# Kernel optimization log

Hardware: AMD Instinct MI355X
Metric: run time of the kernel (lower is better)

The kernel has to match this reference:

```python
import jax, jax.numpy as jnp
import numpy as np
from jax import lax

N, S, K, V, C, D, NH, NB, HD = 4, 1024, 4, 32000, 1000, 512, 8, 6, 2048
DH = D // NH
CAP = round((S // K) * 1.0)  # expert capacity = Seq//K * capacity_factor


def setup_inputs() -> dict:
    key = jax.random.key(0)
    ks = jax.random.split(key, 12)
    nrm = lambda k, shape: jax.random.normal(k, shape, dtype=jnp.float32) * 0.02
    return dict(
        x_in=jax.random.randint(ks[0], (N, S), 0, V),
        y_target=jax.random.randint(ks[1], (N, S), 0, C),
        tok_emb=nrm(ks[2], (K, V, D)),
        pos_emb=nrm(ks[3], (K, S, D)),
        ln1_s=jnp.ones((K, NB, D)), ln1_b=jnp.zeros((K, NB, D)),
        Wqkv=nrm(ks[4], (K, NB, D, 3 * D)), bqkv=jnp.zeros((K, NB, 3 * D)),
        Wo=nrm(ks[5], (K, NB, D, D)), bo=jnp.zeros((K, NB, D)),
        ln2_s=jnp.ones((K, NB, D)), ln2_b=jnp.zeros((K, NB, D)),
        W1=nrm(ks[6], (K, NB, D, HD)), b1=jnp.zeros((K, NB, HD)),
        W2=nrm(ks[7], (K, NB, HD, D)), b2=jnp.zeros((K, NB, D)),
        lnf_s=jnp.ones((K, D)), lnf_b=jnp.zeros((K, D)),
        Wcls=nrm(ks[8], (K, D, C)), bcls=jnp.zeros((K, C)),
        Wconf=nrm(ks[9], (K, D, 1)), bconf=jnp.zeros((K, 1)),
    )


def _ln(x, s, b):
    m = x.mean(-1, keepdims=True)
    v = jnp.var(x, axis=-1, keepdims=True)
    return (x - m) * lax.rsqrt(v + 1e-5) * s + b


def reference(x_in, y_target, tok_emb, pos_emb, ln1_s, ln1_b, Wqkv, bqkv, Wo, bo,
              ln2_s, ln2_b, W1, b1, W2, b2, lnf_s, lnf_b, Wcls, bcls, Wconf, bconf):
    causal = jnp.tril(jnp.ones((S, S), dtype=bool))

    def model_fwd(te, pe, l1s, l1b, wqkv, bq, wo, bo_, l2s, l2b, w1, b1_, w2, b2_, lfs, lfb, wc, bc, wcf, bcf):
        x = te[x_in] + pe[None]  # [N,S,D]
        for i in range(NB):
            h = _ln(x, l1s[i], l1b[i])
            qkv = h @ wqkv[i] + bq[i]
            q, k, v = jnp.split(qkv, 3, axis=-1)
            q = q.reshape(N, S, NH, DH); k = k.reshape(N, S, NH, DH); v = v.reshape(N, S, NH, DH)
            att = jnp.einsum('nqhd,nkhd->nhqk', q, k) / np.float32(np.sqrt(DH))
            att = jax.nn.softmax(jnp.where(causal, att, jnp.float32(-1e9)), axis=-1)
            o = jnp.einsum('nhqk,nkhd->nqhd', att, v).reshape(N, S, D)
            x = x + o @ wo[i] + bo_[i]
            h = _ln(x, l2s[i], l2b[i])
            x = x + jax.nn.gelu(h @ w1[i] + b1_[i]) @ w2[i] + b2_[i]
        x = _ln(x, lfs, lfb)
        return x @ wc + bc, x @ wcf + bcf  # logits [N,S,C], confidence [N,S,1]

    clf, conf = jax.vmap(model_fwd)(tok_emb, pos_emb, ln1_s, ln1_b, Wqkv, bqkv, Wo, bo,
                                    ln2_s, ln2_b, W1, b1, W2, b2, lnf_s, lnf_b, Wcls, bcls, Wconf, bconf)
    combined_classifier = jnp.transpose(clf, (1, 0, 2, 3))       # [N,K,S,C]
    combined_confidence = jnp.transpose(conf[..., 0], (1, 0, 2))  # [N,K,S]

    # --- capacity-constrained auction routing on detached logits ---
    logp = jax.nn.log_softmax(lax.stop_gradient(combined_classifier), axis=-1)
    tgt = jnp.broadcast_to(y_target[:, None, :, None], (N, K, S, 1))
    loss = -jnp.take_along_axis(logp, tgt, axis=-1)[..., 0]  # per-token CE, [N,K,S]
    order = jnp.argsort(loss, axis=1, stable=True)            # [N,K,S] models sorted by loss
    order_s = jnp.transpose(order, (2, 0, 1))                 # [S,N,K]
    rows = jnp.arange(N)

    def step(tc, chunk):  # tc: token_count [N,K]; chunk: [N,K]
        tcm = jnp.take_along_axis(tc, chunk, axis=1)
        best = jnp.argmax((tcm < CAP).astype(jnp.float32), axis=1)
        chosen = chunk[rows, best]
        return tc.at[rows, chosen].add(1.0), chosen

    _, chosen = lax.scan(step, jnp.zeros((N, K), dtype=jnp.float32), order_s)
    activated_models_indices = chosen.T  # [N,S]

    mask = jax.nn.one_hot(activated_models_indices, K, dtype=combined_classifier.dtype)  # [N,S,K]
    mask = jnp.transpose(mask, (0, 2, 1))[..., None]  # [N,K,S,1]
    out = (combined_classifier * mask).sum(axis=1)    # [N,S,C]
    return out, combined_confidence, activated_models_indices
```

## Files before the change

### kernel.cpp

```cpp
#include <hip/hip_runtime.h>
#include <hip/hip_bf16.h>

#define N_  4
#define S_  1024
#define K_  4
#define V_  32000
#define C_  1000
#define D_  512
#define NH_ 8
#define NB_ 6
#define HD_ 2048
#define DH_ 64
#define CAP_ 256
#define M_  (N_*S_)

typedef __attribute__((ext_vector_type(8))) short short8_t;
typedef __attribute__((ext_vector_type(4))) float f32x4_t;

#define MFMA16(a,b,c) __builtin_amdgcn_mfma_f32_16x16x32_bf16((a),(b),(c),0,0,0)

#define HSPLANE ((size_t)M_ * D_)
#define WTMAX   ((size_t)524288)

static __device__ __forceinline__ float bfround(float v) {
    unsigned u = __float_as_uint(v);
    u = (u + 0x7FFFu + ((u >> 16) & 1u)) & 0xFFFF0000u;
    return __uint_as_float(u);
}
static __device__ __forceinline__ void split3(float v, unsigned short& a, unsigned short& b, unsigned short& c) {
    const float f0 = bfround(v);      const float r1 = v - f0;
    const float f1 = bfround(r1);     const float f2 = bfround(r1 - f1);
    a = (unsigned short)(__float_as_uint(f0) >> 16);
    b = (unsigned short)(__float_as_uint(f1) >> 16);
    c = (unsigned short)(__float_as_uint(f2) >> 16);
}
static __device__ __forceinline__ float b2f(unsigned short u) {
    return __uint_as_float((unsigned)u << 16);
}

__global__ __launch_bounds__(256) void embed_kernel(const int* __restrict__ x_in,
    const float* __restrict__ tok, const float* __restrict__ pos, float* __restrict__ x)
{
    const int idx = blockIdx.x * 256 + threadIdx.x;
    const int total = M_ * (D_ / 4);
    if (idx >= total) return;
    const int d = (idx & (D_ / 4 - 1)) * 4;
    const int row = idx >> 7;
    const int s = row & (S_ - 1);
    const int t = x_in[row];
    const float4 a = *(const float4*)(tok + (size_t)t * D_ + d);
    const float4 b = *(const float4*)(pos + (size_t)s * D_ + d);
    float4 r; r.x = a.x + b.x; r.y = a.y + b.y; r.z = a.z + b.z; r.w = a.w + b.w;
    *(float4*)(x + (size_t)row * D_ + d) = r;
}

__global__ __launch_bounds__(256) void ln_kernel(const float* __restrict__ x,
    const float* __restrict__ sc, const float* __restrict__ bi, unsigned short* __restrict__ hs)
{
    const int row = blockIdx.x, tid = threadIdx.x;
    const float* xr = x + (size_t)row * D_;
    float v0 = xr[tid], v1 = xr[tid + 256];
    float s1 = v0 + v1;
#pragma unroll
    for (int off = 32; off; off >>= 1) s1 += __shfl_down(s1, off, 64);
    __shared__ float red[8];
    __shared__ float stat[2];
    const int wid = tid >> 6, lane = tid & 63;
    if (lane == 0) red[wid] = s1;
    __syncthreads();
    if (tid == 0) stat[0] = (red[0] + red[1] + red[2] + red[3]) * (1.f / (float)D_);
    __syncthreads();
    const float mean = stat[0];
    const float d0 = v0 - mean, d1 = v1 - mean;
    float s2 = d0 * d0 + d1 * d1;
#pragma unroll
    for (int off = 32; off; off >>= 1) s2 += __shfl_down(s2, off, 64);
    if (lane == 0) red[wid] = s2;
    __syncthreads();
    if (tid == 0) stat[1] = (red[0] + red[1] + red[2] + red[3]) * (1.f / (float)D_);
    __syncthreads();
    const float rstd = rsqrtf(stat[1] + 1e-5f);
    const float o0 = d0 * rstd * sc[tid] + bi[tid];
    const float o1 = d1 * rstd * sc[tid + 256] + bi[tid + 256];
    unsigned short a, b, c;
    const size_t base = (size_t)row * D_ + tid;
    split3(o0, a, b, c);
    hs[base] = a; hs[base + HSPLANE] = b; hs[base + 2 * HSPLANE] = c;
    split3(o1, a, b, c);
    hs[base + 256] = a; hs[base + 256 + HSPLANE] = b; hs[base + 256 + 2 * HSPLANE] = c;
}

__global__ __launch_bounds__(256) void wsplit_kernel(const float* __restrict__ W, int ldw, int NcTrue,
    unsigned short* __restrict__ Wt, size_t bplane, int Kd)
{
    const int tid = threadIdx.x;
    const int n = blockIdx.x * 64 + (tid & 63);
    const int k0 = blockIdx.y * 32 + (tid >> 6) * 8;
    unsigned short q0[8], q1[8], q2[8];
    if (n < NcTrue) {
#pragma unroll
        for (int j = 0; j < 8; ++j) split3(W[(size_t)(k0 + j) * ldw + n], q0[j], q1[j], q2[j]);
    } else {
#pragma unroll
        for (int j = 0; j < 8; ++j) { q0[j] = 0; q1[j] = 0; q2[j] = 0; }
    }
    unsigned short* dst = Wt + (size_t)n * Kd + k0;
    *(uint4*)dst = *(uint4*)&q0[0];
    *(uint4*)(dst + bplane) = *(uint4*)&q1[0];
    *(uint4*)(dst + 2 * bplane) = *(uint4*)&q2[0];
}

template<int MODE>
__global__ __launch_bounds__(256, 2) void gemm64(const unsigned short* __restrict__ A3, size_t aplane,
    const unsigned short* __restrict__ Bt, size_t bplane, const float* __restrict__ bias,
    void* __restrict__ Cv, size_t cplane, int Nc, int ldc)
{
    constexpr int KD = (MODE == 4) ? 1024 : 512;
    __shared__ __align__(16) unsigned short Bs[3][64][40];
    const int tid = threadIdx.x;
    const int gx = gridDim.x;
    const int nwg = gx * gridDim.y;
    const int bid = blockIdx.y * gx + blockIdx.x;
    const int cpx = nwg >> 3;
    const int swz = (bid & 7) * cpx + (bid >> 3);
    const int bm = (swz / gx) * 128, bn = (swz % gx) * 64;
    const int wid = tid >> 6, lane = tid & 63;
    const int wm = (wid >> 1) * 64, wn = (wid & 1) * 32;
    const int lr = lane & 15, lg = lane >> 4;
    const int scol = tid >> 2, skq = tid & 3;
    const unsigned short* Bp0 = Bt + (size_t)(bn + scol) * KD + skq * 8;
    const unsigned short* Ap0 = A3 + (size_t)(bm + wm + lr) * KD + lg * 8;

    f32x4_t acc[4][2] = {};

#pragma unroll
    for (int k0 = 0; k0 < KD; k0 += 32) {
        const uint4 bq0 = *(const uint4*)(Bp0 + k0);
        const uint4 bq1 = *(const uint4*)(Bp0 + bplane + k0);
        const uint4 bq2 = *(const uint4*)(Bp0 + 2 * bplane + k0);
        short8_t af[3][4];
#pragma unroll
        for (int m = 0; m < 4; ++m) {
            const unsigned short* ap = Ap0 + (size_t)m * 16 * KD + k0;
            af[0][m] = *(const short8_t*)ap;
            af[1][m] = *(const short8_t*)(ap + aplane);
            af[2][m] = *(const short8_t*)(ap + 2 * aplane);
        }
        __syncthreads();
        *(uint4*)&Bs[0][scol][skq * 8] = bq0;
        *(uint4*)&Bs[1][scol][skq * 8] = bq1;
        *(uint4*)&Bs[2][scol][skq * 8] = bq2;
        __syncthreads();
        short8_t bg[3][2];
#pragma unroll
        for (int s = 0; s < 3; ++s)
#pragma unroll
            for (int n2 = 0; n2 < 2; ++n2)
                bg[s][n2] = *(const short8_t*)&Bs[s][wn + n2 * 16 + lr][lg * 8];
#pragma unroll
        for (int m = 0; m < 4; ++m)
#pragma unroll
            for (int n2 = 0; n2 < 2; ++n2) {
                f32x4_t c = acc[m][n2];
                c = MFMA16(af[0][m], bg[0][n2], c);
                c = MFMA16(af[0][m], bg[1][n2], c);
                c = MFMA16(af[1][m], bg[0][n2], c);
                c = MFMA16(af[1][m], bg[1][n2], c);
                c = MFMA16(af[0][m], bg[2][n2], c);
                c = MFMA16(af[2][m], bg[0][n2], c);
                acc[m][n2] = c;
            }
    }
#pragma unroll
    for (int m = 0; m < 4; ++m)
#pragma unroll
        for (int n2 = 0; n2 < 2; ++n2) {
            const int col = bn + wn + n2 * 16 + lr;
            if (col >= Nc) continue;
            const float bv = bias ? bias[col] : 0.f;
            const int row0 = bm + wm + m * 16 + lg * 4;
#pragma unroll
            for (int r = 0; r < 4; ++r) {
                float v = acc[m][n2][r] + bv;
                if (MODE == 2) {
                    const float t = v;
                    v = 0.5f * t * (1.f + tanhf(0.7978845608028654f * (t + 0.044715f * t * t * t)));
                    unsigned short a, b, c;
                    split3(v, a, b, c);
                    unsigned short* Cp = (unsigned short*)Cv + (size_t)(row0 + r) * ldc + col;
                    Cp[0] = a; Cp[cplane] = b; Cp[2 * cplane] = c;
                } else {
                    float* cp = (float*)Cv + (size_t)(row0 + r) * ldc + col;
                    if (MODE == 1 || MODE == 4) v += *cp;
                    *cp = v;
                }
            }
        }
}

__global__ __launch_bounds__(256) void rerun_kernel(const unsigned short* __restrict__ A,
    const unsigned short* __restrict__ B0, const float* __restrict__ bias,
    const int* __restrict__ chosen, const int kk, float* __restrict__ out)
{
    __shared__ int anyrow;
    const int tid = threadIdx.x;
    const int bm = blockIdx.y * 128, bn = blockIdx.x * 64;
    if (tid == 0) anyrow = 0;
    __syncthreads();
    if (tid < 128 && chosen[bm + tid] == kk) anyrow = 1;
    __syncthreads();
    if (!anyrow) return;
    const int wid = tid >> 6, lane = tid & 63;
    const int wm = (wid >> 1) * 64, wn = (wid & 1) * 32;
    const int lr = lane & 15, lg = lane >> 4;
    f32x4_t acc[4][2] = {};
#pragma unroll
    for (int k0 = 0; k0 < D_; k0 += 32) {
        short8_t af[4], bg[2];
#pragma unroll
        for (int m = 0; m < 4; ++m)
            af[m] = *(const short8_t*)(A + (size_t)(bm + wm + m * 16 + lr) * D_ + k0 + lg * 8);
#pragma unroll
        for (int n2 = 0; n2 < 2; ++n2)
            bg[n2] = *(const short8_t*)(B0 + (size_t)(bn + wn + n2 * 16 + lr) * D_ + k0 + lg * 8);
#pragma unroll
        for (int m = 0; m < 4; ++m)
#pragma unroll
            for (int n2 = 0; n2 < 2; ++n2)
                acc[m][n2] = MFMA16(af[m], bg[n2], acc[m][n2]);
    }
#pragma unroll
    for (int m = 0; m < 4; ++m)
#pragma unroll
        for (int n2 = 0; n2 < 2; ++n2) {
            const int col = bn + wn + n2 * 16 + lr;
            if (col >= C_) continue;
            const float bv = bias[col];
            const int row0 = bm + wm + m * 16 + lg * 4;
#pragma unroll
            for (int r = 0; r < 4; ++r) {
                const int row = row0 + r;
                if (chosen[row] == kk) out[(size_t)row * C_ + col] = acc[m][n2][r] + bv;
            }
        }
}

__global__ __launch_bounds__(256) void attn_mfma_kernel(const float* __restrict__ qkv, unsigned short* __restrict__ hsO)
{
    __shared__ __align__(16) unsigned short Ks[3][32][72];
    __shared__ __align__(16) unsigned short Vt[3][64][40];
    __shared__ __align__(16) unsigned short Ps[4][3][16][40];
    const int qt = blockIdx.x, hh = blockIdx.y, n = blockIdx.z;
    const int tid = threadIdx.x;
    const int w = tid >> 6, lane = tid & 63;
    const int lr = lane & 15, lg = lane >> 4;
    const size_t rs = 3 * D_;
    const float* base = qkv + (size_t)n * S_ * rs + hh * DH_;

    short8_t qf[3][2];
    {
        const int qrow = qt * 64 + w * 16 + lr;
#pragma unroll
        for (int ks = 0; ks < 2; ++ks) {
            const float* qp = base + (size_t)qrow * rs + ks * 32 + lg * 8;
            float v[8];
            *(float4*)&v[0] = ((const float4*)qp)[0];
            *(float4*)&v[4] = ((const float4*)qp)[1];
#pragma unroll
            for (int j = 0; j < 8; ++j) {
                unsigned short a, b, c;
                split3(v[j], a, b, c);
                qf[0][ks][j] = (short)a; qf[1][ks][j] = (short)b; qf[2][ks][j] = (short)c;
            }
        }
    }

    f32x4_t oacc[4] = {};
    float m_r[4], l_r[4];
#pragma unroll
    for (int r = 0; r < 4; ++r) { m_r[r] = -1e30f; l_r[r] = 0.f; }

    const int ktmax = 2 * qt + 2;
    for (int kt = 0; kt < ktmax; ++kt) {
        __syncthreads();
        {
            const int key = tid & 31, seg = tid >> 5;
            const float* kp = base + (size_t)(kt * 32 + key) * rs + D_ + seg * 8;
            const float* vp = kp + D_;
            float kv[8], vv[8];
            *(float4*)&kv[0] = ((const float4*)kp)[0];
            *(float4*)&kv[4] = ((const float4*)kp)[1];
            *(float4*)&vv[0] = ((const float4*)vp)[0];
            *(float4*)&vv[4] = ((const float4*)vp)[1];
            unsigned short k0a[8], k1a[8], k2a[8];
#pragma unroll
            for (int j = 0; j < 8; ++j) split3(kv[j], k0a[j], k1a[j], k2a[j]);
            *(uint4*)&Ks[0][key][seg * 8] = *(uint4*)&k0a[0];
            *(uint4*)&Ks[1][key][seg * 8] = *(uint4*)&k1a[0];
            *(uint4*)&Ks[2][key][seg * 8] = *(uint4*)&k2a[0];
#pragma unroll
            for (int j = 0; j < 8; ++j) {
                unsigned short a, b, c;
                split3(vv[j], a, b, c);
                Vt[0][seg * 8 + j][key] = a;
                Vt[1][seg * 8 + j][key] = b;
                Vt[2][seg * 8 + j][key] = c;
            }
        }
        __syncthreads();
        f32x4_t sacc[2] = {};
#pragma unroll
        for (int n2 = 0; n2 < 2; ++n2) {
#pragma unroll
            for (int ks = 0; ks < 2; ++ks) {
                short8_t kb0 = *(const short8_t*)&Ks[0][n2 * 16 + lr][ks * 32 + lg * 8];
                short8_t kb1 = *(const short8_t*)&Ks[1][n2 * 16 + lr][ks * 32 + lg * 8];
                short8_t kb2 = *(const short8_t*)&Ks[2][n2 * 16 + lr][ks * 32 + lg * 8];
                f32x4_t c = sacc[n2];
                c = MFMA16(qf[0][ks], kb0, c);
                c = MFMA16(qf[0][ks], kb1, c);
                c = MFMA16(qf[1][ks], kb0, c);
                c = MFMA16(qf[1][ks], kb1, c);
                c = MFMA16(qf[0][ks], kb2, c);
                c = MFMA16(qf[2][ks], kb0, c);
                sacc[n2] = c;
            }
        }
        float p[2][4];
#pragma unroll
        for (int n2 = 0; n2 < 2; ++n2)
#pragma unroll
            for (int r = 0; r < 4; ++r) {
                float s = sacc[n2][r] * 0.125f;
                const int key = kt * 32 + n2 * 16 + lr;
                const int qrow = qt * 64 + w * 16 + lg * 4 + r;
                if (key > qrow) s = -1e30f;
                p[n2][r] = s;
            }
        float scl[4];
#pragma unroll
        for (int r = 0; r < 4; ++r) {
            float tm = fmaxf(p[0][r], p[1][r]);
            tm = fmaxf(tm, __shfl_xor(tm, 1));
            tm = fmaxf(tm, __shfl_xor(tm, 2));
            tm = fmaxf(tm, __shfl_xor(tm, 4));
            tm = fmaxf(tm, __shfl_xor(tm, 8));
            const float mnew = fmaxf(m_r[r], tm);
            scl[r] = expf(m_r[r] - mnew);
            m_r[r] = mnew;
        }
#pragma unroll
        for (int r = 0; r < 4; ++r) {
            p[0][r] = expf(p[0][r] - m_r[r]);
            p[1][r] = expf(p[1][r] - m_r[r]);
            float ts = p[0][r] + p[1][r];
            ts += __shfl_xor(ts, 1);
            ts += __shfl_xor(ts, 2);
            ts += __shfl_xor(ts, 4);
            ts += __shfl_xor(ts, 8);
            l_r[r] = l_r[r] * scl[r] + ts;
        }
#pragma unroll
        for (int nf = 0; nf < 4; ++nf)
#pragma unroll
            for (int r = 0; r < 4; ++r) oacc[nf][r] *= scl[r];
#pragma unroll
        for (int n2 = 0; n2 < 2; ++n2)
#pragma unroll
            for (int r = 0; r < 4; ++r) {
                unsigned short a, b, c;
                split3(p[n2][r], a, b, c);
                Ps[w][0][lg * 4 + r][n2 * 16 + lr] = a;
                Ps[w][1][lg * 4 + r][n2 * 16 + lr] = b;
                Ps[w][2][lg * 4 + r][n2 * 16 + lr] = c;
            }
        short8_t pa0 = *(const short8_t*)&Ps[w][0][lr][lg * 8];
        short8_t pa1 = *(const short8_t*)&Ps[w][1][lr][lg * 8];
        short8_t pa2 = *(const short8_t*)&Ps[w][2][lr][lg * 8];
#pragma unroll
        for (int nf = 0; nf < 4; ++nf) {
            short8_t vb0 = *(const short8_t*)&Vt[0][nf * 16 + lr][lg * 8];
            short8_t vb1 = *(const short8_t*)&Vt[1][nf * 16 + lr][lg * 8];
            short8_t vb2 = *(const short8_t*)&Vt[2][nf * 16 + lr][lg * 8];
            f32x4_t c = oacc[nf];
            c = MFMA16(pa0, vb0, c);
            c = MFMA16(pa0, vb1, c);
            c = MFMA16(pa1, vb0, c);
            c = MFMA16(pa1, vb1, c);
            c = MFMA16(pa0, vb2, c);
            c = MFMA16(pa2, vb0, c);
            oacc[nf] = c;
        }
    }
    float inv[4];
#pragma unroll
    for (int r = 0; r < 4; ++r) inv[r] = 1.f / l_r[r];
#pragma unroll
    for (int nf = 0; nf < 4; ++nf)
#pragma unroll
        for (int r = 0; r < 4; ++r) {
            const int qrow = qt * 64 + w * 16 + lg * 4 + r;
            const size_t idx = ((size_t)n * S_ + qrow) * D_ + hh * DH_ + nf * 16 + lr;
            unsigned short a, b, c;
            split3(oacc[nf][r] * inv[r], a, b, c);
            hsO[idx] = a; hsO[idx + HSPLANE] = b; hsO[idx + 2 * HSPLANE] = c;
        }
}

__global__ __launch_bounds__(256) void copy_kernel(const unsigned short* __restrict__ src,
    unsigned short* __restrict__ dst)
{
    const int idx = blockIdx.x * 256 + threadIdx.x;
    if (idx >= M_ * D_ / 8) return;
    ((uint4*)dst)[idx] = ((const uint4*)src)[idx];
}

__global__ __launch_bounds__(256) void conf_kernel(const unsigned short* __restrict__ hs,
    const float* __restrict__ w, const float* __restrict__ bc, float* __restrict__ conf_out, int k)
{
    const int wid = threadIdx.x >> 6, lane = threadIdx.x & 63;
    const int row = blockIdx.x * 4 + wid;
    const unsigned short* h0 = hs + (size_t)row * D_;
    const unsigned short* h1 = h0 + HSPLANE;
    float sm = 0.f;
#pragma unroll
    for (int j = 0; j < 8; ++j) {
        const int i = lane + 64 * j;
        sm += (b2f(h0[i]) + b2f(h1[i])) * w[i];
    }
#pragma unroll
    for (int off = 32; off; off >>= 1) sm += __shfl_down(sm, off, 64);
    if (lane == 0) {
        const int n = row >> 10, s = row & (S_ - 1);
        conf_out[((size_t)n * K_ + k) * S_ + s] = sm + bc[0];
    }
}

__global__ __launch_bounds__(256) void loss_kernel(const float* __restrict__ logits,
    const int* __restrict__ y, float* __restrict__ loss)
{
    const int row = blockIdx.x;
    const float* lr = logits + (size_t)row * C_;
    const int tid = threadIdx.x;
    __shared__ float red[256];
    float mx = -1e30f;
    for (int c = tid; c < C_; c += 256) mx = fmaxf(mx, lr[c]);
    red[tid] = mx; __syncthreads();
    for (int st = 128; st > 0; st >>= 1) {
        if (tid < st) red[tid] = fmaxf(red[tid], red[tid + st]);
        __syncthreads();
    }
    mx = red[0];
    __syncthreads();
    float sm = 0.f;
    for (int c = tid; c < C_; c += 256) sm += expf(lr[c] - mx);
    red[tid] = sm; __syncthreads();
    for (int st = 128; st > 0; st >>= 1) {
        if (tid < st) red[tid] += red[tid + st];
        __syncthreads();
    }
    if (tid == 0) loss[row] = logf(red[0]) + mx - lr[y[row]];
}

__global__ __launch_bounds__(256) void routing_kernel(const float* __restrict__ loss,
    float* __restrict__ idx_out, int* __restrict__ chosen_buf)
{
    __shared__ float l_s[K_][S_];
    __shared__ unsigned char ord_s[S_];
    const int n = blockIdx.x;
    const int tid = threadIdx.x;
#pragma unroll
    for (int k = 0; k < K_; ++k)
        ((float4*)l_s[k])[tid] = ((const float4*)(loss + (size_t)k * M_ + n * S_))[tid];
    __syncthreads();
    for (int s = tid; s < S_; s += 256) {
        float l[K_];
#pragma unroll
        for (int k = 0; k < K_; ++k) l[k] = l_s[k][s];
        int ord[K_] = {0, 1, 2, 3};
#pragma unroll
        for (int i = 1; i < K_; ++i) {
            const int v = ord[i];
            int j = i;
            while (j > 0 && l[ord[j - 1]] > l[v]) { ord[j] = ord[j - 1]; --j; }
            ord[j] = v;
        }
        ord_s[s] = (unsigned char)(ord[0] | (ord[1] << 2) | (ord[2] << 4) | (ord[3] << 6));
    }
    __syncthreads();
    if (tid == 0) {
        int tc[K_] = {0, 0, 0, 0};
        for (int s = 0; s < S_; ++s) {
            const unsigned b = ord_s[s];
            int ch = b & 3;
#pragma unroll
            for (int j = 0; j < K_; ++j) {
                const int m = (b >> (2 * j)) & 3;
                if (tc[m] < CAP_) { ch = m; break; }
            }
            ++tc[ch];
            chosen_buf[n * S_ + s] = ch;
            idx_out[n * S_ + s] = (float)ch;
        }
    }
}

extern "C" void kernel_launch(void* const* d_in, const int* in_sizes, int n_in,
                              void* d_out, int out_size, void* d_ws, size_t ws_size,
                              hipStream_t stream)
{
    const int*   x_in = (const int*)d_in[0];
    const int*   y    = (const int*)d_in[1];
    const float* tok  = (const float*)d_in[2];
    const float* pos  = (const float*)d_in[3];
    const float* ln1s = (const float*)d_in[4];
    const float* ln1b = (const float*)d_in[5];
    const float* Wqkv = (const float*)d_in[6];
    const float* bqkv = (const float*)d_in[7];
    const float* Wo   = (const float*)d_in[8];
    const float* bo   = (const float*)d_in[9];
    const float* ln2s = (const float*)d_in[10];
    const float* ln2b = (const float*)d_in[11];
    const float* W1   = (const float*)d_in[12];
    const float* b1   = (const float*)d_in[13];
    const float* W2   = (const float*)d_in[14];
    const float* b2   = (const float*)d_in[15];
    const float* lnfs = (const float*)d_in[16];
    const float* lnfb = (const float*)d_in[17];
    const float* Wcls = (const float*)d_in[18];
    const float* bcls = (const float*)d_in[19];
    const float* Wcnf = (const float*)d_in[20];
    const float* bcnf = (const float*)d_in[21];

    if (ws_size < 66142208) return;
    float* R = (float*)d_ws;
    unsigned short* hs   = (unsigned short*)(R + (size_t)M_ * 1536);
    float* x             = (float*)(hs + 3 * HSPLANE);
    unsigned short* hfin = (unsigned short*)(x + (size_t)M_ * D_);
    unsigned short* Wt   = hfin + (size_t)K_ * M_ * D_;
    float* loss          = (float*)(Wt + 3 * WTMAX);
    int*   chosen        = (int*)(loss + (size_t)K_ * M_);
    unsigned short* mids = (unsigned short*)R;
    const size_t midplane = (size_t)M_ * 1024;

    float* out      = (float*)d_out;
    float* conf_out = out + (size_t)M_ * C_;
    float* idx_out  = conf_out + (size_t)N_ * K_ * S_;

    for (int k = 0; k < K_; ++k) {
        embed_kernel<<<(M_ * (D_ / 4) + 255) / 256, 256, 0, stream>>>(
            x_in, tok + (size_t)k * V_ * D_, pos + (size_t)k * S_ * D_, x);
        for (int i = 0; i < NB_; ++i) {
            const size_t ki = (size_t)k * NB_ + i;
            ln_kernel<<<M_, 256, 0, stream>>>(x, ln1s + ki * D_, ln1b + ki * D_, hs);
            for (int c = 0; c < 2; ++c) {
                wsplit_kernel<<<dim3(12, 16), 256, 0, stream>>>(
                    Wqkv + ki * D_ * 3 * D_ + c * 768, 3 * D_, 768, Wt, 768 * 512, D_);
                gemm64<0><<<dim3(12, 32), 256, 0, stream>>>(
                    hs, HSPLANE, Wt, 768 * 512, bqkv + ki * 3 * D_ + c * 768,
                    R + c * 768, 0, 768, 3 * D_);
            }
            attn_mfma_kernel<<<dim3(S_ / 64, NH_, N_), 256, 0, stream>>>(R, hs);
            wsplit_kernel<<<dim3(8, 16), 256, 0, stream>>>(Wo + ki * D_ * D_, D_, D_, Wt, 512 * 512, D_);
            gemm64<1><<<dim3(8, 32), 256, 0, stream>>>(
                hs, HSPLANE, Wt, 512 * 512, bo + ki * D_, x, 0, D_, D_);
            ln_kernel<<<M_, 256, 0, stream>>>(x, ln2s + ki * D_, ln2b + ki * D_, hs);
            for (int c = 0; c < 2; ++c) {
                wsplit_kernel<<<dim3(16, 16), 256, 0, stream>>>(
                    W1 + ki * D_ * HD_ + c * 1024, HD_, 1024, Wt, 1024 * 512, D_);
                gemm64<2><<<dim3(16, 32), 256, 0, stream>>>(
                    hs, HSPLANE, Wt, 1024 * 512, b1 + ki * HD_ + c * 1024,
                    mids, midplane, 1024, 1024);
                wsplit_kernel<<<dim3(8, 32), 256, 0, stream>>>(
                    W2 + ki * HD_ * D_ + (size_t)c * 1024 * D_, D_, D_, Wt, 512 * 1024, 1024);
                gemm64<4><<<dim3(8, 32), 256, 0, stream>>>(
                    mids, midplane, Wt, 512 * 1024, (c == 0) ? (b2 + ki * D_) : nullptr,
                    x, 0, D_, D_);
            }
        }
        ln_kernel<<<M_, 256, 0, stream>>>(x, lnfs + (size_t)k * D_, lnfb + (size_t)k * D_, hs);
        copy_kernel<<<(M_ * D_ / 8 + 255) / 256, 256, 0, stream>>>(hs, hfin + (size_t)k * M_ * D_);
        wsplit_kernel<<<dim3(16, 16), 256, 0, stream>>>(
            Wcls + (size_t)k * D_ * C_, C_, C_, Wt, 1024 * 512, D_);
        gemm64<0><<<dim3(16, 32), 256, 0, stream>>>(
            hs, HSPLANE, Wt, 1024 * 512, bcls + (size_t)k * C_, R, 0, C_, C_);
        conf_kernel<<<M_ / 4, 256, 0, stream>>>(hs, Wcnf + (size_t)k * D_, bcnf + k, conf_out, k);
        loss_kernel<<<M_, 256, 0, stream>>>(R, y, loss + (size_t)k * M_);
    }
    routing_kernel<<<N_, 256, 0, stream>>>(loss, idx_out, chosen);
    for (int k = 0; k < K_; ++k) {
        wsplit_kernel<<<dim3(16, 16), 256, 0, stream>>>(
            Wcls + (size_t)k * D_ * C_, C_, C_, Wt, 1024 * 512, D_);
        rerun_kernel<<<dim3(16, 32), 256, 0, stream>>>(
            hfin + (size_t)k * M_ * D_, Wt, bcls + (size_t)k * C_, chosen, k, out);
    }
}
```

Measured before the change: 13.80 ms.

## Add 128x128 split-bf16 GEMM tile and fuse final LN with hfin copy

Adds a new GEMM kernel, gemm_t2, that uses 128x128 output tiles with a register-prefetched single LDS buffer and runs the six split-bf16 product segments as separate K sweeps. The QKV, FFN1 and classifier GEMMs now use it with half as many blocks. This is meant to raise arithmetic intensity and reduce reloads of A and B. The final layernorm now writes the hi plane straight into hfin, which removes a separate copy kernel. gemm64 is simplified to accumulate-only, since only modes 1 and 4 still use it. The larger tiles lower occupancy, and the segment-outer loop adds a barrier-heavy reload pass for each segment.

```diff
diff --git a/kernel.cpp b/kernel.cpp
--- a/kernel.cpp
+++ b/kernel.cpp
@@ -54,8 +54,10 @@
     *(float4*)(x + (size_t)row * D_ + d) = r;
 }
 
+template<int FIN>
 __global__ __launch_bounds__(256) void ln_kernel(const float* __restrict__ x,
-    const float* __restrict__ sc, const float* __restrict__ bi, unsigned short* __restrict__ hs)
+    const float* __restrict__ sc, const float* __restrict__ bi, unsigned short* __restrict__ hs,
+    unsigned short* __restrict__ hfin)
 {
     const int row = blockIdx.x, tid = threadIdx.x;
     const float* xr = x + (size_t)row * D_;
@@ -86,8 +88,10 @@
     const size_t base = (size_t)row * D_ + tid;
     split3(o0, a, b, c);
     hs[base] = a; hs[base + HSPLANE] = b; hs[base + 2 * HSPLANE] = c;
+    if (FIN) hfin[base] = a;
     split3(o1, a, b, c);
     hs[base + 256] = a; hs[base + 256 + HSPLANE] = b; hs[base + 256 + 2 * HSPLANE] = c;
+    if (FIN) hfin[base + 256] = a;
 }
 
 __global__ __launch_bounds__(256) void wsplit_kernel(const float* __restrict__ W, int ldw, int NcTrue,
@@ -108,6 +112,86 @@
     *(uint4*)dst = *(uint4*)&q0[0];
     *(uint4*)(dst + bplane) = *(uint4*)&q1[0];
     *(uint4*)(dst + 2 * bplane) = *(uint4*)&q2[0];
+}
+
+template<int MODE>
+__global__ __launch_bounds__(256) void gemm_t2(const unsigned short* __restrict__ A3, size_t aplane,
+    const unsigned short* __restrict__ Bt, size_t bplane, const float* __restrict__ bias,
+    void* __restrict__ Cv, size_t cplane, int Nc, int ldc)
+{
+    constexpr int KD = 512;
+    __shared__ __align__(16) unsigned short As[128][40];
+    __shared__ __align__(16) unsigned short Bs[128][40];
+    const int tid = threadIdx.x;
+    const int bm = blockIdx.y * 128, bn = blockIdx.x * 128;
+    const int wid = tid >> 6, lane = tid & 63;
+    const int wm = (wid >> 1) * 64, wn = (wid & 1) * 64;
+    const int lr = lane & 15, lg = lane >> 4;
+    const int srow = tid >> 1, sof = (tid & 1) * 16;
+
+    const unsigned short* ApB = A3 + (size_t)(bm + srow) * KD + sof;
+    const unsigned short* BpB = Bt + (size_t)(bn + srow) * KD + sof;
+
+    f32x4_t acc[4][4] = {};
+    const int SA[6] = {0, 0, 1, 1, 0, 2};
+    const int SB[6] = {0, 1, 0, 1, 2, 0};
+
+    for (int seg = 0; seg < 6; ++seg) {
+        const unsigned short* Ap = ApB + (size_t)SA[seg] * aplane;
+        const unsigned short* Bp = BpB + (size_t)SB[seg] * bplane;
+        uint4 pa0 = *(const uint4*)(Ap);
+        uint4 pa1 = *(const uint4*)(Ap + 8);
+        uint4 pb0 = *(const uint4*)(Bp);
+        uint4 pb1 = *(const uint4*)(Bp + 8);
+#pragma unroll
+        for (int k0 = 0; k0 < KD; k0 += 32) {
+            __syncthreads();
+            *(uint4*)&As[srow][sof]     = pa0;
+            *(uint4*)&As[srow][sof + 8] = pa1;
+            *(uint4*)&Bs[srow][sof]     = pb0;
+            *(uint4*)&Bs[srow][sof + 8] = pb1;
+            __syncthreads();
+            if (k0 + 32 < KD) {
+                pa0 = *(const uint4*)(Ap + k0 + 32);
+                pa1 = *(const uint4*)(Ap + k0 + 40);
+                pb0 = *(const uint4*)(Bp + k0 + 32);
+                pb1 = *(const uint4*)(Bp + k0 + 40);
+            }
+            short8_t af[4], bf[4];
+#pragma unroll
+            for (int m = 0; m < 4; ++m) af[m] = *(const short8_t*)&As[wm + m * 16 + lr][lg * 8];
+#pragma unroll
+            for (int n = 0; n < 4; ++n) bf[n] = *(const short8_t*)&Bs[wn + n * 16 + lr][lg * 8];
+#pragma unroll
+            for (int m = 0; m < 4; ++m)
+#pragma unroll
+                for (int n = 0; n < 4; ++n)
+                    acc[m][n] = MFMA16(af[m], bf[n], acc[m][n]);
+        }
+    }
+#pragma unroll
+    for (int m = 0; m < 4; ++m)
+#pragma unroll
+        for (int n = 0; n < 4; ++n) {
+            const int col = bn + wn + n * 16 + lr;
+            if (col >= Nc) continue;
+            const float bv = bias ? bias[col] : 0.f;
+            const int row0 = bm + wm + m * 16 + lg * 4;
+#pragma unroll
+            for (int r = 0; r < 4; ++r) {
+                float v = acc[m][n][r] + bv;
+                if (MODE == 2) {
+                    const float t = v;
+                    v = 0.5f * t * (1.f + tanhf(0.7978845608028654f * (t + 0.044715f * t * t * t)));
+                    unsigned short a, b, c;
+                    split3(v, a, b, c);
+                    unsigned short* Cp = (unsigned short*)Cv + (size_t)(row0 + r) * ldc + col;
+                    Cp[0] = a; Cp[cplane] = b; Cp[2 * cplane] = c;
+                } else {
+                    ((float*)Cv)[(size_t)(row0 + r) * ldc + col] = v;
+                }
+            }
+        }
 }
 
 template<int MODE>
@@ -181,19 +265,8 @@
             const int row0 = bm + wm + m * 16 + lg * 4;
 #pragma unroll
             for (int r = 0; r < 4; ++r) {
-                float v = acc[m][n2][r] + bv;
-                if (MODE == 2) {
-                    const float t = v;
-                    v = 0.5f * t * (1.f + tanhf(0.7978845608028654f * (t + 0.044715f * t * t * t)));
-                    unsigned short a, b, c;
-                    split3(v, a, b, c);
-                    unsigned short* Cp = (unsigned short*)Cv + (size_t)(row0 + r) * ldc + col;
-                    Cp[0] = a; Cp[cplane] = b; Cp[2 * cplane] = c;
-                } else {
-                    float* cp = (float*)Cv + (size_t)(row0 + r) * ldc + col;
-                    if (MODE == 1 || MODE == 4) v += *cp;
-                    *cp = v;
-                }
+                float* cp = (float*)Cv + (size_t)(row0 + r) * ldc + col;
+                *cp = *cp + acc[m][n2][r] + bv;
             }
         }
 }
@@ -405,14 +478,6 @@
             split3(oacc[nf][r] * inv[r], a, b, c);
             hsO[idx] = a; hsO[idx + HSPLANE] = b; hsO[idx + 2 * HSPLANE] = c;
         }
-}
-
-__global__ __launch_bounds__(256) void copy_kernel(const unsigned short* __restrict__ src,
-    unsigned short* __restrict__ dst)
-{
-    const int idx = blockIdx.x * 256 + threadIdx.x;
-    if (idx >= M_ * D_ / 8) return;
-    ((uint4*)dst)[idx] = ((const uint4*)src)[idx];
 }
 
 __global__ __launch_bounds__(256) void conf_kernel(const unsigned short* __restrict__ hs,
@@ -552,11 +617,11 @@
             x_in, tok + (size_t)k * V_ * D_, pos + (size_t)k * S_ * D_, x);
         for (int i = 0; i < NB_; ++i) {
             const size_t ki = (size_t)k * NB_ + i;
-            ln_kernel<<<M_, 256, 0, stream>>>(x, ln1s + ki * D_, ln1b + ki * D_, hs);
+            ln_kernel<0><<<M_, 256, 0, stream>>>(x, ln1s + ki * D_, ln1b + ki * D_, hs, nullptr);
             for (int c = 0; c < 2; ++c) {
                 wsplit_kernel<<<dim3(12, 16), 256, 0, stream>>>(
                     Wqkv + ki * D_ * 3 * D_ + c * 768, 3 * D_, 768, Wt, 768 * 512, D_);
-                gemm64<0><<<dim3(12, 32), 256, 0, stream>>>(
+                gemm_t2<0><<<dim3(6, 32), 256, 0, stream>>>(
                     hs, HSPLANE, Wt, 768 * 512, bqkv + ki * 3 * D_ + c * 768,
                     R + c * 768, 0, 768, 3 * D_);
             }
@@ -564,11 +629,11 @@
             wsplit_kernel<<<dim3(8, 16), 256, 0, stream>>>(Wo + ki * D_ * D_, D_, D_, Wt, 512 * 512, D_);
             gemm64<1><<<dim3(8, 32), 256, 0, stream>>>(
                 hs, HSPLANE, Wt, 512 * 512, bo + ki * D_, x, 0, D_, D_);
-            ln_kernel<<<M_, 256, 0, stream>>>(x, ln2s + ki * D_, ln2b + ki * D_, hs);
+            ln_kernel<0><<<M_, 256, 0, stream>>>(x, ln2s + ki * D_, ln2b + ki * D_, hs, nullptr);
             for (int c = 0; c < 2; ++c) {
                 wsplit_kernel<<<dim3(16, 16), 256, 0, stream>>>(
                     W1 + ki * D_ * HD_ + c * 1024, HD_, 1024, Wt, 1024 * 512, D_);
-                gemm64<2><<<dim3(16, 32), 256, 0, stream>>>(
+                gemm_t2<2><<<dim3(8, 32), 256, 0, stream>>>(
                     hs, HSPLANE, Wt, 1024 * 512, b1 + ki * HD_ + c * 1024,
                     mids, midplane, 1024, 1024);
                 wsplit_kernel<<<dim3(8, 32), 256, 0, stream>>>(
@@ -578,11 +643,11 @@
                     x, 0, D_, D_);
             }
         }
-        ln_kernel<<<M_, 256, 0, stream>>>(x, lnfs + (size_t)k * D_, lnfb + (size_t)k * D_, hs);
-        copy_kernel<<<(M_ * D_ / 8 + 255) / 256, 256, 0, stream>>>(hs, hfin + (size_t)k * M_ * D_);
+        ln_kernel<1><<<M_, 256, 0, stream>>>(x, lnfs + (size_t)k * D_, lnfb + (size_t)k * D_,
+                                             hs, hfin + (size_t)k * M_ * D_);
         wsplit_kernel<<<dim3(16, 16), 256, 0, stream>>>(
             Wcls + (size_t)k * D_ * C_, C_, C_, Wt, 1024 * 512, D_);
-        gemm64<0><<<dim3(16, 32), 256, 0, stream>>>(
+        gemm_t2<0><<<dim3(8, 32), 256, 0, stream>>>(
             hs, HSPLANE, Wt, 1024 * 512, bcls + (size_t)k * C_, R, 0, C_, C_);
         conf_kernel<<<M_ / 4, 256, 0, stream>>>(hs, Wcnf + (size_t)k * D_, bcnf + k, conf_out, k);
         loss_kernel<<<M_, 256, 0, stream>>>(R, y, loss + (size_t)k * M_);
```

Result: slower. 15.60 ms (+13.1%).

## Fuse weight bf16 split into GEMM B-tile loads and drop copy kernel

Applied to the files above, without the earlier changes.

Removes the separate wsplit kernel that pre-split fp32 weights into three bf16 planes. Each GEMM now reads the fp32 weights directly and splits them in registers while staging the B tile, and QKV runs as a single GEMM launch instead of two. The final LayerNorm writes hfin directly, which removes the copy kernel, and the rerun kernel converts the classifier weights itself. This cuts launches and global round trips for the transformed weights. In exchange, each GEMM block redoes the split work, and the fp32 weight reads are strided column loads that coalesce less well than the earlier pre-transposed layout.

```diff
diff --git a/kernel.cpp b/kernel.cpp
--- a/kernel.cpp
+++ b/kernel.cpp
@@ -20,7 +20,6 @@
 #define MFMA16(a,b,c) __builtin_amdgcn_mfma_f32_16x16x32_bf16((a),(b),(c),0,0,0)
 
 #define HSPLANE ((size_t)M_ * D_)
-#define WTMAX   ((size_t)524288)
 
 static __device__ __forceinline__ float bfround(float v) {
     unsigned u = __float_as_uint(v);
@@ -33,6 +32,10 @@
     a = (unsigned short)(__float_as_uint(f0) >> 16);
     b = (unsigned short)(__float_as_uint(f1) >> 16);
     c = (unsigned short)(__float_as_uint(f2) >> 16);
+}
+static __device__ __forceinline__ unsigned short f2bf(float f) {
+    unsigned u = __float_as_uint(f);
+    return (unsigned short)((u + 0x7FFFu + ((u >> 16) & 1u)) >> 16);
 }
 static __device__ __forceinline__ float b2f(unsigned short u) {
     return __uint_as_float((unsigned)u << 16);
@@ -54,8 +57,10 @@
     *(float4*)(x + (size_t)row * D_ + d) = r;
 }
 
+template<int FIN>
 __global__ __launch_bounds__(256) void ln_kernel(const float* __restrict__ x,
-    const float* __restrict__ sc, const float* __restrict__ bi, unsigned short* __restrict__ hs)
+    const float* __restrict__ sc, const float* __restrict__ bi, unsigned short* __restrict__ hs,
+    unsigned short* __restrict__ hfin)
 {
     const int row = blockIdx.x, tid = threadIdx.x;
     const float* xr = x + (size_t)row * D_;
@@ -86,33 +91,15 @@
     const size_t base = (size_t)row * D_ + tid;
     split3(o0, a, b, c);
     hs[base] = a; hs[base + HSPLANE] = b; hs[base + 2 * HSPLANE] = c;
+    if (FIN) hfin[base] = a;
     split3(o1, a, b, c);
     hs[base + 256] = a; hs[base + 256 + HSPLANE] = b; hs[base + 256 + 2 * HSPLANE] = c;
-}
-
-__global__ __launch_bounds__(256) void wsplit_kernel(const float* __restrict__ W, int ldw, int NcTrue,
-    unsigned short* __restrict__ Wt, size_t bplane, int Kd)
-{
-    const int tid = threadIdx.x;
-    const int n = blockIdx.x * 64 + (tid & 63);
-    const int k0 = blockIdx.y * 32 + (tid >> 6) * 8;
-    unsigned short q0[8], q1[8], q2[8];
-    if (n < NcTrue) {
-#pragma unroll
-        for (int j = 0; j < 8; ++j) split3(W[(size_t)(k0 + j) * ldw + n], q0[j], q1[j], q2[j]);
-    } else {
-#pragma unroll
-        for (int j = 0; j < 8; ++j) { q0[j] = 0; q1[j] = 0; q2[j] = 0; }
-    }
-    unsigned short* dst = Wt + (size_t)n * Kd + k0;
-    *(uint4*)dst = *(uint4*)&q0[0];
-    *(uint4*)(dst + bplane) = *(uint4*)&q1[0];
-    *(uint4*)(dst + 2 * bplane) = *(uint4*)&q2[0];
+    if (FIN) hfin[base + 256] = a;
 }
 
 template<int MODE>
-__global__ __launch_bounds__(256, 2) void gemm64(const unsigned short* __restrict__ A3, size_t aplane,
-    const unsigned short* __restrict__ Bt, size_t bplane, const float* __restrict__ bias,
+__global__ __launch_bounds__(256, 2) void gemm64f(const unsigned short* __restrict__ A3, size_t aplane,
+    const float* __restrict__ Bf, int ldb, const float* __restrict__ bias,
     void* __restrict__ Cv, size_t cplane, int Nc, int ldc)
 {
     constexpr int KD = (MODE == 4) ? 1024 : 512;
@@ -128,16 +115,24 @@
     const int wm = (wid >> 1) * 64, wn = (wid & 1) * 32;
     const int lr = lane & 15, lg = lane >> 4;
     const int scol = tid >> 2, skq = tid & 3;
-    const unsigned short* Bp0 = Bt + (size_t)(bn + scol) * KD + skq * 8;
+    const int gcol = bn + scol;
     const unsigned short* Ap0 = A3 + (size_t)(bm + wm + lr) * KD + lg * 8;
 
     f32x4_t acc[4][2] = {};
 
 #pragma unroll
     for (int k0 = 0; k0 < KD; k0 += 32) {
-        const uint4 bq0 = *(const uint4*)(Bp0 + k0);
-        const uint4 bq1 = *(const uint4*)(Bp0 + bplane + k0);
-        const uint4 bq2 = *(const uint4*)(Bp0 + 2 * bplane + k0);
+        float bv[8];
+        if (gcol < Nc) {
+#pragma unroll
+            for (int j = 0; j < 8; ++j) bv[j] = Bf[(size_t)(k0 + skq * 8 + j) * ldb + gcol];
+        } else {
+#pragma unroll
+            for (int j = 0; j < 8; ++j) bv[j] = 0.f;
+        }
+        unsigned short q0[8], q1[8], q2[8];
+#pragma unroll
+        for (int j = 0; j < 8; ++j) split3(bv[j], q0[j], q1[j], q2[j]);
         short8_t af[3][4];
 #pragma unroll
         for (int m = 0; m < 4; ++m) {
@@ -147,9 +142,9 @@
             af[2][m] = *(const short8_t*)(ap + 2 * aplane);
         }
         __syncthreads();
-        *(uint4*)&Bs[0][scol][skq * 8] = bq0;
-        *(uint4*)&Bs[1][scol][skq * 8] = bq1;
-        *(uint4*)&Bs[2][scol][skq * 8] = bq2;
+        *(uint4*)&Bs[0][scol][skq * 8] = *(uint4*)&q0[0];
+        *(uint4*)&Bs[1][scol][skq * 8] = *(uint4*)&q1[0];
+        *(uint4*)&Bs[2][scol][skq * 8] = *(uint4*)&q2[0];
         __syncthreads();
         short8_t bg[3][2];
 #pragma unroll
@@ -199,7 +194,7 @@
 }
 
 __global__ __launch_bounds__(256) void rerun_kernel(const unsigned short* __restrict__ A,
-    const unsigned short* __restrict__ B0, const float* __restrict__ bias,
+    const float* __restrict__ Wc, const float* __restrict__ bias,
     const int* __restrict__ chosen, const int kk, float* __restrict__ out)
 {
     __shared__ int anyrow;
@@ -221,8 +216,17 @@
         for (int m = 0; m < 4; ++m)
             af[m] = *(const short8_t*)(A + (size_t)(bm + wm + m * 16 + lr) * D_ + k0 + lg * 8);
 #pragma unroll
-        for (int n2 = 0; n2 < 2; ++n2)
-            bg[n2] = *(const short8_t*)(B0 + (size_t)(bn + wn + n2 * 16 + lr) * D_ + k0 + lg * 8);
+        for (int n2 = 0; n2 < 2; ++n2) {
+            const int col = bn + wn + n2 * 16 + lr;
+            if (col < C_) {
+#pragma unroll
+                for (int j = 0; j < 8; ++j)
+                    bg[n2][j] = (short)f2bf(Wc[(size_t)(k0 + lg * 8 + j) * C_ + col]);
+            } else {
+#pragma unroll
+                for (int j = 0; j < 8; ++j) bg[n2][j] = 0;
+            }
+        }
 #pragma unroll
         for (int m = 0; m < 4; ++m)
 #pragma unroll
@@ -405,14 +409,6 @@
             split3(oacc[nf][r] * inv[r], a, b, c);
             hsO[idx] = a; hsO[idx + HSPLANE] = b; hsO[idx + 2 * HSPLANE] = c;
         }
-}
-
-__global__ __launch_bounds__(256) void copy_kernel(const unsigned short* __restrict__ src,
-    unsigned short* __restrict__ dst)
-{
-    const int idx = blockIdx.x * 256 + threadIdx.x;
-    if (idx >= M_ * D_ / 8) return;
-    ((uint4*)dst)[idx] = ((const uint4*)src)[idx];
 }
 
 __global__ __launch_bounds__(256) void conf_kernel(const unsigned short* __restrict__ hs,
@@ -538,7 +534,7 @@
     float* x             = (float*)(hs + 3 * HSPLANE);
     unsigned short* hfin = (unsigned short*)(x + (size_t)M_ * D_);
     unsigned short* Wt   = hfin + (size_t)K_ * M_ * D_;
-    float* loss          = (float*)(Wt + 3 * WTMAX);
+    float* loss          = (float*)(Wt + 3 * (size_t)524288);
     int*   chosen        = (int*)(loss + (size_t)K_ * M_);
     unsigned short* mids = (unsigned short*)R;
     const size_t midplane = (size_t)M_ * 1024;
@@ -552,46 +548,33 @@
             x_in, tok + (size_t)k * V_ * D_, pos + (size_t)k * S_ * D_, x);
         for (int i = 0; i < NB_; ++i) {
             const size_t ki = (size_t)k * NB_ + i;
-            ln_kernel<<<M_, 256, 0, stream>>>(x, ln1s + ki * D_, ln1b + ki * D_, hs);
+            ln_kernel<0><<<M_, 256, 0, stream>>>(x, ln1s + ki * D_, ln1b + ki * D_, hs, nullptr);
+            gemm64f<0><<<dim3(24, 32), 256, 0, stream>>>(
+                hs, HSPLANE, Wqkv + ki * D_ * 3 * D_, 3 * D_, bqkv + ki * 3 * D_,
+                R, 0, 3 * D_, 3 * D_);
+            attn_mfma_kernel<<<dim3(S_ / 64, NH_, N_), 256, 0, stream>>>(R, hs);
+            gemm64f<1><<<dim3(8, 32), 256, 0, stream>>>(
+                hs, HSPLANE, Wo + ki * D_ * D_, D_, bo + ki * D_, x, 0, D_, D_);
+            ln_kernel<0><<<M_, 256, 0, stream>>>(x, ln2s + ki * D_, ln2b + ki * D_, hs, nullptr);
             for (int c = 0; c < 2; ++c) {
-                wsplit_kernel<<<dim3(12, 16), 256, 0, stream>>>(
-                    Wqkv + ki * D_ * 3 * D_ + c * 768, 3 * D_, 768, Wt, 768 * 512, D_);
-                gemm64<0><<<dim3(12, 32), 256, 0, stream>>>(
-                    hs, HSPLANE, Wt, 768 * 512, bqkv + ki * 3 * D_ + c * 768,
-                    R + c * 768, 0, 768, 3 * D_);
-            }
-            attn_mfma_kernel<<<dim3(S_ / 64, NH_, N_), 256, 0, stream>>>(R, hs);
-            wsplit_kernel<<<dim3(8, 16), 256, 0, stream>>>(Wo + ki * D_ * D_, D_, D_, Wt, 512 * 512, D_);
-            gemm64<1><<<dim3(8, 32), 256, 0, stream>>>(
-                hs, HSPLANE, Wt, 512 * 512, bo + ki * D_, x, 0, D_, D_);
-            ln_kernel<<<M_, 256, 0, stream>>>(x, ln2s + ki * D_, ln2b + ki * D_, hs);
-            for (int c = 0; c < 2; ++c) {
-                wsplit_kernel<<<dim3(16, 16), 256, 0, stream>>>(
-                    W1 + ki * D_ * HD_ + c * 1024, HD_, 1024, Wt, 1024 * 512, D_);
-                gemm64<2><<<dim3(16, 32), 256, 0, stream>>>(
-                    hs, HSPLANE, Wt, 1024 * 512, b1 + ki * HD_ + c * 1024,
+                gemm64f<2><<<dim3(16, 32), 256, 0, stream>>>(
+                    hs, HSPLANE, W1 + ki * D_ * HD_ + c * 1024, HD_, b1 + ki * HD_ + c * 1024,
                     mids, midplane, 1024, 1024);
-                wsplit_kernel<<<dim3(8, 32), 256, 0, stream>>>(
-                    W2 + ki * HD_ * D_ + (size_t)c * 1024 * D_, D_, D_, Wt, 512 * 1024, 1024);
-                gemm64<4><<<dim3(8, 32), 256, 0, stream>>>(
-                    mids, midplane, Wt, 512 * 1024, (c == 0) ? (b2 + ki * D_) : nullptr,
-                    x, 0, D_, D_);
-            }
-        }
-        ln_kernel<<<M_, 256, 0, stream>>>(x, lnfs + (size_t)k * D_, lnfb + (size_t)k * D_, hs);
-        copy_kernel<<<(M_ * D_ / 8 + 255) / 256, 256, 0, stream>>>(hs, hfin + (size_t)k * M_ * D_);
-        wsplit_kernel<<<dim3(16, 16), 256, 0, stream>>>(
-            Wcls + (size_t)k * D_ * C_, C_, C_, Wt, 1024 * 512, D_);
-        gemm64<0><<<dim3(16, 32), 256, 0, stream>>>(
-            hs, HSPLANE, Wt, 1024 * 512, bcls + (size_t)k * C_, R, 0, C_, C_);
+                gemm64f<4><<<dim3(8, 32), 256, 0, stream>>>(
+                    mids, midplane, W2 + ki * HD_ * D_ + (size_t)c * 1024 * D_, D_,
+                    (c == 0) ? (b2 + ki * D_) : nullptr, x, 0, D_, D_);
+            }
+        }
+        ln_kernel<1><<<M_, 256, 0, stream>>>(x, lnfs + (size_t)k * D_, lnfb + (size_t)k * D_,
+                                             hs, hfin + (size_t)k * M_ * D_);
+        gemm64f<0><<<dim3(16, 32), 256, 0, stream>>>(
+            hs, HSPLANE, Wcls + (size_t)k * D_ * C_, C_, bcls + (size_t)k * C_, R, 0, C_, C_);
         conf_kernel<<<M_ / 4, 256, 0, stream>>>(hs, Wcnf + (size_t)k * D_, bcnf + k, conf_out, k);
         loss_kernel<<<M_, 256, 0, stream>>>(R, y, loss + (size_t)k * M_);
     }
     routing_kernel<<<N_, 256, 0, stream>>>(loss, idx_out, chosen);
-    for (int k = 0; k < K_; ++k) {
-        wsplit_kernel<<<dim3(16, 16), 256, 0, stream>>>(
-            Wcls + (size_t)k * D_ * C_, C_, C_, Wt, 1024 * 512, D_);
+    for (int k = 0; k < K_; ++k)
         rerun_kernel<<<dim3(16, 32), 256, 0, stream>>>(
-            hfin + (size_t)k * M_ * D_, Wt, bcls + (size_t)k * C_, chosen, k, out);
-    }
-}
+            hfin + (size_t)k * M_ * D_, Wcls + (size_t)k * D_ * C_, bcls + (size_t)k * C_,
+            chosen, k, out);
+}
```

Result: faster. 13.53 ms (-2.0%).
